# Optimization experiments

Measured on AMD Instinct MI355X. Metric: run time of the kernel, lower is better.

The kernel has to match this reference:

```python
import jax, jax.numpy as jnp
import numpy as np

D = 1024
H = 16
DH = D // H  # 64
FF_H = 4096
EPS = 1e-5


def layernorm(x, gamma, beta):
    mu = jnp.mean(x, axis=-1, keepdims=True)
    var = jnp.var(x, axis=-1, keepdims=True)
    return (x - mu) * jax.lax.rsqrt(var + EPS) * gamma + beta


def setup_inputs() -> dict:
    key = jax.random.key(0)
    ks = jax.random.split(key, 12)
    B, S = 2, 2048
    q = jax.random.normal(ks[0], (B, S, D), dtype=jnp.float32)
    k = jax.random.normal(ks[1], (B, S, D), dtype=jnp.float32)
    v = jax.random.normal(ks[2], (B, S, D), dtype=jnp.float32)
    time_lengths = jax.random.randint(ks[3], (B,), 0, S)
    mask = jnp.zeros((1, 1, S, S), dtype=jnp.float32)
    sc = 0.02
    Wq = jax.random.normal(ks[4], (D, D), dtype=jnp.float32) * sc
    Wk = jax.random.normal(ks[5], (D, D), dtype=jnp.float32) * sc
    Wv = jax.random.normal(ks[6], (D, D), dtype=jnp.float32) * sc
    Wd = jax.random.normal(ks[7], (D, D), dtype=jnp.float32) * sc
    W1 = jax.random.normal(ks[8], (D, FF_H), dtype=jnp.float32) * sc
    b1 = jnp.zeros((FF_H,), dtype=jnp.float32)
    W2 = jax.random.normal(ks[9], (FF_H, D), dtype=jnp.float32) * sc
    b2 = jnp.zeros((D,), dtype=jnp.float32)
    g1 = jnp.ones((D,), dtype=jnp.float32)
    be1 = jnp.zeros((D,), dtype=jnp.float32)
    g2 = jnp.ones((D,), dtype=jnp.float32)
    be2 = jnp.zeros((D,), dtype=jnp.float32)
    return {"q": q, "k": k, "v": v, "time_lengths": time_lengths, "mask": mask,
            "Wq": Wq, "Wk": Wk, "Wv": Wv, "Wd": Wd,
            "W1": W1, "b1": b1, "W2": W2, "b2": b2,
            "g1": g1, "be1": be1, "g2": g2, "be2": be2}


def reference(q, k, v, time_lengths, mask, Wq, Wk, Wv, Wd, W1, b1, W2, b2, g1, be1, g2, be2):
    B, S, _ = q.shape
    scale = jnp.sqrt(jnp.float32(DH))
    # project and split heads: [B,H,S,DH]
    qh = (q @ Wq).reshape(B, S, H, DH).transpose(0, 2, 1, 3)
    kh = (k @ Wk).reshape(B, S, H, DH).transpose(0, 2, 1, 3)
    vh = (v @ Wv).reshape(B, S, H, DH).transpose(0, 2, 1, 3)
    score = jnp.einsum('bhqd,bhkd->bhqk', qh, kh) / scale + mask
    attn = jax.nn.softmax(score, axis=-1)
    z = jnp.einsum('bhqk,bhkd->bhqd', attn, vh)
    z = z.transpose(0, 2, 1, 3).reshape(B, S, D)
    z = z @ Wd
    # Add & LayerNorm 1 (note: original applies LN to attn out, then adds q)
    x = layernorm(z, g1, be1) + q
    # FF (dropout is identity in eval)
    ff = jax.nn.relu(x @ W1 + b1) @ W2 + b2
    return layernorm(ff + x, g2, be2)
```

## Files before the change

### kernel.cpp

```cpp
#include <hip/hip_runtime.h>
#include <hip/hip_bf16.h>


#define SEQ 2048
#define DM  1024
#define LNEPS 1e-5f

typedef __attribute__((ext_vector_type(8))) short bf16x8;
typedef __attribute__((ext_vector_type(4))) float f32x4;

#define GAS __attribute__((address_space(1)))
#define LAS __attribute__((address_space(3)))

static __device__ __forceinline__ void gl_lds16(const unsigned short* g, unsigned short* l) {
    __builtin_amdgcn_global_load_lds((const GAS void*)g, (LAS void*)l, 16, 0, 0);
}

static __device__ __forceinline__ unsigned short f2bf(float f) {
    unsigned u = __builtin_bit_cast(unsigned, f);
    u += 0x7fffu + ((u >> 16) & 1u);
    return (unsigned short)(u >> 16);
}

__global__ __launch_bounds__(256) void gemm_bf16(
    const unsigned short* __restrict__ A, const unsigned short* __restrict__ Bt,
    float* __restrict__ Cf, unsigned short* __restrict__ Cb,
    int M, int N, int Klen, int lda, int ldb,
    size_t sA, size_t sB, size_t sC,
    const float* __restrict__ bias, int ep)
{
    __shared__ unsigned short As[128 * 32];
    __shared__ unsigned short Bs[128 * 32];

    const int t = threadIdx.x, lane = t & 63, w = t >> 6;
    const int wm = w >> 1, wn = w & 1;
    const int m0 = blockIdx.y * 128, n0 = blockIdx.x * 128;
    A  += (size_t)blockIdx.z * sA;
    Bt += (size_t)blockIdx.z * sB;
    const size_t cbase = (size_t)blockIdx.z * sC;
    const int l15 = lane & 15, l16 = lane >> 4;
    const int ar = lane >> 2, ac = (lane & 3) * 8;

    f32x4 acc[4][4];
    #pragma unroll
    for (int i = 0; i < 4; i++)
        #pragma unroll
        for (int j = 0; j < 4; j++)
            acc[i][j] = (f32x4){0.f, 0.f, 0.f, 0.f};

    for (int k0 = 0; k0 < Klen; k0 += 32) {
        __syncthreads();
        #pragma unroll
        for (int i = 0; i < 2; i++) {
            const int rg = w * 2 + i;
            gl_lds16(&A [(size_t)(m0 + rg * 16 + ar) * lda + k0 + ac], &As[rg * 512]);
            gl_lds16(&Bt[(size_t)(n0 + rg * 16 + ar) * ldb + k0 + ac], &Bs[rg * 512]);
        }
        __syncthreads();

        bf16x8 af[4], bfr[4];
        #pragma unroll
        for (int i = 0; i < 4; i++) {
            af[i]  = *(const bf16x8*)&As[(wm * 64 + i * 16 + l15) * 32 + l16 * 8];
            bfr[i] = *(const bf16x8*)&Bs[(wn * 64 + i * 16 + l15) * 32 + l16 * 8];
        }
        #pragma unroll
        for (int mi = 0; mi < 4; mi++)
            #pragma unroll
            for (int ni = 0; ni < 4; ni++)
                acc[mi][ni] = __builtin_amdgcn_mfma_f32_16x16x32_bf16(
                    af[mi], bfr[ni], acc[mi][ni], 0, 0, 0);
    }

    #pragma unroll
    for (int ni = 0; ni < 4; ni++) {
        const int col = n0 + wn * 64 + ni * 16 + l15;
        const float bv = (ep && blockIdx.z == 0) ? bias[col] : 0.f;
        #pragma unroll
        for (int mi = 0; mi < 4; mi++) {
            #pragma unroll
            for (int r = 0; r < 4; r++) {
                const int row = m0 + wm * 64 + mi * 16 + l16 * 4 + r;
                float vv = acc[mi][ni][r] + bv;
                if (ep == 2) vv = fmaxf(vv, 0.f);
                if (Cf) Cf[cbase + (size_t)row * N + col] = vv;
                else    Cb[cbase + (size_t)row * N + col] = f2bf(vv);
            }
        }
    }
}

__global__ __launch_bounds__(256) void attn_mfma(
    const unsigned short* __restrict__ qh, const unsigned short* __restrict__ kh,
    const unsigned short* __restrict__ vhT, const float* __restrict__ mask,
    unsigned short* __restrict__ z)
{
    __shared__ unsigned short Qs[64 * 64];
    __shared__ unsigned short Ks[64 * 64];
    __shared__ unsigned short Vst[64 * 64];
    __shared__ unsigned short Ps[64 * 72];

    const int t = threadIdx.x, lane = t & 63, w = t >> 6;
    const int bid = blockIdx.x;
    const int qt = bid >> 5, h = bid & 15, b = (bid >> 4) & 1;
    const int q0 = qt * 64, qr = w * 16;
    const int l15 = lane & 15, l16 = lane >> 4;

    const int lr = lane >> 3;
    const int gc = ((lane & 7) ^ lr) * 8;

    const size_t qbase = (size_t)(b * SEQ + q0) * DM + h * 64;
    const size_t kbase = (size_t)(b * SEQ) * DM + h * 64;
    const size_t vbase = (size_t)((b * 16 + h) * 64) * SEQ;

    #pragma unroll
    for (int i = 0; i < 2; i++) {
        const int rg = w * 2 + i;
        gl_lds16(&qh[qbase + (size_t)(rg * 8 + lr) * DM + gc], &Qs[rg * 512]);
    }
    __syncthreads();

    const int sw0 = ((l16    ) ^ (l15 & 7)) * 8;
    const int sw1 = ((l16 + 4) ^ (l15 & 7)) * 8;
    const bf16x8 bQ0 = *(const bf16x8*)&Qs[(qr + l15) * 64 + sw0];
    const bf16x8 bQ1 = *(const bf16x8*)&Qs[(qr + l15) * 64 + sw1];

    const float* mrow = mask + (size_t)(q0 + qr + l15) * SEQ;

    float m_i = -1e30f, l_i = 0.f;
    f32x4 o4[4];
    #pragma unroll
    for (int mi = 0; mi < 4; mi++) o4[mi] = (f32x4){0.f, 0.f, 0.f, 0.f};

    for (int kt = 0; kt < SEQ / 64; kt++) {
        const int k0 = kt * 64;
        __syncthreads();
        #pragma unroll
        for (int i = 0; i < 2; i++) {
            const int rg = w * 2 + i;
            gl_lds16(&kh [kbase + (size_t)(k0 + rg * 8 + lr) * DM + gc], &Ks[rg * 512]);
            gl_lds16(&vhT[vbase + (size_t)(rg * 8 + lr) * SEQ + k0 + gc], &Vst[rg * 512]);
        }
        __syncthreads();

        f32x4 s4[4];
        #pragma unroll
        for (int ki = 0; ki < 4; ki++) {
            const int r = ki * 16 + l15;
            const bf16x8 aK0 = *(const bf16x8*)&Ks[r * 64 + sw0];
            const bf16x8 aK1 = *(const bf16x8*)&Ks[r * 64 + sw1];
            f32x4 a0 = (f32x4){0.f, 0.f, 0.f, 0.f};
            a0 = __builtin_amdgcn_mfma_f32_16x16x32_bf16(aK0, bQ0, a0, 0, 0, 0);
            s4[ki] = __builtin_amdgcn_mfma_f32_16x16x32_bf16(aK1, bQ1, a0, 0, 0, 0);
        }

        float sv[4][4];
        #pragma unroll
        for (int ki = 0; ki < 4; ki++) {
            const float4 mv = *(const float4*)&mrow[k0 + ki * 16 + l16 * 4];
            sv[ki][0] = s4[ki][0] * 0.125f + mv.x;
            sv[ki][1] = s4[ki][1] * 0.125f + mv.y;
            sv[ki][2] = s4[ki][2] * 0.125f + mv.z;
            sv[ki][3] = s4[ki][3] * 0.125f + mv.w;
        }

        float rm = -1e30f;
        #pragma unroll
        for (int ki = 0; ki < 4; ki++)
            #pragma unroll
            for (int r = 0; r < 4; r++) rm = fmaxf(rm, sv[ki][r]);
        rm = fmaxf(rm, __shfl_xor(rm, 16));
        rm = fmaxf(rm, __shfl_xor(rm, 32));
        const float mnew  = fmaxf(m_i, rm);
        const float alpha = __expf(m_i - mnew);
        m_i = mnew;

        float ps = 0.f;
        #pragma unroll
        for (int ki = 0; ki < 4; ki++) {
            float p[4];
            #pragma unroll
            for (int r = 0; r < 4; r++) { p[r] = __expf(sv[ki][r] - mnew); ps += p[r]; }
            ushort4 pk;
            pk.x = f2bf(p[0]); pk.y = f2bf(p[1]); pk.z = f2bf(p[2]); pk.w = f2bf(p[3]);
            *(ushort4*)&Ps[(qr + l15) * 72 + ki * 16 + l16 * 4] = pk;
        }
        ps += __shfl_xor(ps, 16);
        ps += __shfl_xor(ps, 32);
        l_i = l_i * alpha + ps;
        #pragma unroll
        for (int mi = 0; mi < 4; mi++)
            #pragma unroll
            for (int r = 0; r < 4; r++) o4[mi][r] *= alpha;

        const bf16x8 bP0 = *(const bf16x8*)&Ps[(qr + l15) * 72 + l16 * 8];
        const bf16x8 bP1 = *(const bf16x8*)&Ps[(qr + l15) * 72 + 32 + l16 * 8];
        #pragma unroll
        for (int mi = 0; mi < 4; mi++) {
            const int r = mi * 16 + l15;
            const bf16x8 aV0 = *(const bf16x8*)&Vst[r * 64 + sw0];
            const bf16x8 aV1 = *(const bf16x8*)&Vst[r * 64 + sw1];
            o4[mi] = __builtin_amdgcn_mfma_f32_16x16x32_bf16(aV0, bP0, o4[mi], 0, 0, 0);
            o4[mi] = __builtin_amdgcn_mfma_f32_16x16x32_bf16(aV1, bP1, o4[mi], 0, 0, 0);
        }
    }

    const float inv = 1.f / l_i;
    #pragma unroll
    for (int mi = 0; mi < 4; mi++) {
        ushort4 ok;
        ok.x = f2bf(o4[mi][0] * inv); ok.y = f2bf(o4[mi][1] * inv);
        ok.z = f2bf(o4[mi][2] * inv); ok.w = f2bf(o4[mi][3] * inv);
        *(ushort4*)&z[(size_t)(b * SEQ + q0 + qr + l15) * DM + h * 64 + mi * 16 + l16 * 4] = ok;
    }
}

__global__ __launch_bounds__(256) void cast3_bf16(
    const float* __restrict__ a0, const float* __restrict__ a1, const float* __restrict__ a2,
    unsigned short* __restrict__ out)
{
    const float* src = blockIdx.z == 0 ? a0 : (blockIdx.z == 1 ? a1 : a2);
    const size_t i = ((size_t)blockIdx.x * 256 + threadIdx.x) * 4;
    const float4 v = *(const float4*)&src[i];
    ushort4 o; o.x = f2bf(v.x); o.y = f2bf(v.y); o.z = f2bf(v.z); o.w = f2bf(v.w);
    *(ushort4*)&out[(size_t)blockIdx.z * ((size_t)SEQ * 2 * DM) + i] = o;
}

__global__ __launch_bounds__(256) void transpose_cast(
    const float* __restrict__ W, unsigned short* __restrict__ Wt, int K, int N)
{
    __shared__ float ts[64][65];
    const int n0 = blockIdx.x * 64, k0 = blockIdx.y * 64;
    const int t = threadIdx.x, r = t >> 4, c4 = (t & 15) * 4;
    #pragma unroll
    for (int i = 0; i < 4; i++) {
        const float4 v = *(const float4*)&W[(size_t)(k0 + r + i * 16) * N + n0 + c4];
        ts[r + i * 16][c4 + 0] = v.x; ts[r + i * 16][c4 + 1] = v.y;
        ts[r + i * 16][c4 + 2] = v.z; ts[r + i * 16][c4 + 3] = v.w;
    }
    __syncthreads();
    #pragma unroll
    for (int i = 0; i < 4; i++) {
        const int n = r + i * 16;
        ushort4 o;
        o.x = f2bf(ts[c4 + 0][n]); o.y = f2bf(ts[c4 + 1][n]);
        o.z = f2bf(ts[c4 + 2][n]); o.w = f2bf(ts[c4 + 3][n]);
        *(ushort4*)&Wt[(size_t)(n0 + n) * K + k0 + c4] = o;
    }
}

__global__ __launch_bounds__(256) void transpose_v(
    const unsigned short* __restrict__ vh, unsigned short* __restrict__ vhT)
{
    __shared__ unsigned short ts[64][80];
    const int s0 = blockIdx.x * 64, h = blockIdx.y, b = blockIdx.z;
    const int t = threadIdx.x, rr = t >> 3, c8 = (t & 7) * 8;
    #pragma unroll
    for (int i = 0; i < 2; i++) {
        const int srow = rr + i * 32;
        *(uint4*)&ts[srow][c8] = *(const uint4*)&vh[(size_t)(b * SEQ + s0 + srow) * DM + h * 64 + c8];
    }
    __syncthreads();
    #pragma unroll
    for (int i = 0; i < 2; i++) {
        const int dr = rr + i * 32;
        ushort4 ov0, ov1;
        ov0.x = ts[c8 + 0][dr]; ov0.y = ts[c8 + 1][dr];
        ov0.z = ts[c8 + 2][dr]; ov0.w = ts[c8 + 3][dr];
        ov1.x = ts[c8 + 4][dr]; ov1.y = ts[c8 + 5][dr];
        ov1.z = ts[c8 + 6][dr]; ov1.w = ts[c8 + 7][dr];
        *(ushort4*)&vhT[(size_t)((b * 16 + h) * 64 + dr) * SEQ + s0 + c8] = ov0;
        *(ushort4*)&vhT[(size_t)((b * 16 + h) * 64 + dr) * SEQ + s0 + c8 + 4] = ov1;
    }
}

__global__ __launch_bounds__(256) void ln_res(
    const float* __restrict__ a, const float* __restrict__ a2,
    const float* __restrict__ r,
    const float* __restrict__ g, const float* __restrict__ be,
    float* __restrict__ out, unsigned short* __restrict__ outb, int mode)
{
    __shared__ float redls[8];
    const int row = blockIdx.x, t = threadIdx.x;
    const size_t base = (size_t)row * DM;

    float vals[4], s = 0.f, sq = 0.f;
    #pragma unroll
    for (int i = 0; i < 4; i++) {
        const int c = t + 256 * i;
        float x = a[base + c];
        if (a2) x += a2[base + c];
        if (mode == 1) x += r[base + c];
        vals[i] = x; s += x; sq += x * x;
    }
    #pragma unroll
    for (int off = 32; off > 0; off >>= 1) { s += __shfl_down(s, off); sq += __shfl_down(sq, off); }
    if ((t & 63) == 0) { redls[t >> 6] = s; redls[4 + (t >> 6)] = sq; }
    __syncthreads();
    s  = redls[0] + redls[1] + redls[2] + redls[3];
    sq = redls[4] + redls[5] + redls[6] + redls[7];

    const float mu  = s * (1.f / 1024.f);
    const float var = sq * (1.f / 1024.f) - mu * mu;
    const float rs  = rsqrtf(var + LNEPS);
    #pragma unroll
    for (int i = 0; i < 4; i++) {
        const int c = t + 256 * i;
        float y = (vals[i] - mu) * rs * g[c] + be[c];
        if (mode == 0) y += r[base + c];
        out[base + c] = y;
        if (outb) outb[base + c] = f2bf(y);
    }
}

extern "C" void kernel_launch(void* const* d_in, const int* in_sizes, int n_in,
                              void* d_out, int out_size, void* d_ws, size_t ws_size,
                              hipStream_t stream)
{
    const float* q    = (const float*)d_in[0];
    const float* k    = (const float*)d_in[1];
    const float* v    = (const float*)d_in[2];
    const float* mask = (const float*)d_in[4];
    const float* Wq   = (const float*)d_in[5];
    const float* Wk   = (const float*)d_in[6];
    const float* Wv   = (const float*)d_in[7];
    const float* Wd   = (const float*)d_in[8];
    const float* W1   = (const float*)d_in[9];
    const float* b1   = (const float*)d_in[10];
    const float* W2   = (const float*)d_in[11];
    const float* b2   = (const float*)d_in[12];
    const float* g1   = (const float*)d_in[13];
    const float* be1  = (const float*)d_in[14];
    const float* g2   = (const float*)d_in[15];
    const float* be2  = (const float*)d_in[16];
    float* out = (float*)d_out;

    char* WS = (char*)d_ws;
    const size_t MiB = 1u << 20;
    const size_t ND  = (size_t)4096 * 1024;

    unsigned short* qb  = (unsigned short*)(WS + 0);
    unsigned short* vhT = (unsigned short*)(WS + 0);
    unsigned short* zb  = (unsigned short*)(WS + 8 * MiB);
    unsigned short* xb  = (unsigned short*)(WS + 16 * MiB);
    unsigned short* Wqt = (unsigned short*)(WS + 24 * MiB);
    unsigned short* Wdt = (unsigned short*)(WS + 30 * MiB);
    unsigned short* W1t = (unsigned short*)(WS + 32 * MiB);
    unsigned short* W2t = (unsigned short*)(WS + 40 * MiB);
    unsigned short* qh  = (unsigned short*)(WS + 48 * MiB);
    float*          zd0 = (float*)(WS + 48 * MiB);
    float*          zd1 = (float*)(WS + 64 * MiB);
    float*          x   = (float*)(WS + 80 * MiB);
    unsigned short* h1  = (unsigned short*)(WS + 96 * MiB);
    float*          y0  = (float*)(WS + 48 * MiB);
    float*          y1  = (float*)(WS + 64 * MiB);

    unsigned short* kh = qh + ND;
    unsigned short* vh = qh + 2 * ND;

    const dim3 blk(256);

    cast3_bf16<<<dim3(4096, 1, 3), blk, 0, stream>>>(q, k, v, qb);
    transpose_cast<<<dim3(16, 16), blk, 0, stream>>>(Wq, Wqt,                   1024, 1024);
    transpose_cast<<<dim3(16, 16), blk, 0, stream>>>(Wk, Wqt + 1024 * 1024,     1024, 1024);
    transpose_cast<<<dim3(16, 16), blk, 0, stream>>>(Wv, Wqt + 2 * 1024 * 1024, 1024, 1024);
    transpose_cast<<<dim3(16, 16), blk, 0, stream>>>(Wd, Wdt, 1024, 1024);
    transpose_cast<<<dim3(64, 16), blk, 0, stream>>>(W1, W1t, 1024, 4096);
    transpose_cast<<<dim3(16, 64), blk, 0, stream>>>(W2, W2t, 4096, 1024);

    gemm_bf16<<<dim3(8, 32, 3), blk, 0, stream>>>(qb, Wqt, nullptr, qh,
        4096, 1024, 1024, 1024, 1024, ND, (size_t)1024 * 1024, ND, nullptr, 0);

    transpose_v<<<dim3(32, 16, 2), blk, 0, stream>>>(vh, vhT);

    attn_mfma<<<dim3(1024), blk, 0, stream>>>(qh, kh, vhT, mask, zb);

    gemm_bf16<<<dim3(8, 32, 2), blk, 0, stream>>>(zb, Wdt, zd0, nullptr,
        4096, 1024, 512, 1024, 1024, 512, 512, ND, nullptr, 0);

    ln_res<<<dim3(4096), blk, 0, stream>>>(zd0, zd1, q, g1, be1, x, xb, 0);

    gemm_bf16<<<dim3(32, 32, 1), blk, 0, stream>>>(xb, W1t, nullptr, h1,
        4096, 4096, 1024, 1024, 1024, 0, 0, 0, b1, 2);
    gemm_bf16<<<dim3(8, 32, 2), blk, 0, stream>>>(h1, W2t, y0, nullptr,
        4096, 1024, 2048, 4096, 4096, 2048, 2048, ND, b2, 1);

    ln_res<<<dim3(4096), blk, 0, stream>>>(y0, y1, x, g2, be2, out, nullptr, 1);
}
```

Before: 504.0 us.

## Double-buffer K tiles in attention with manual vmcnt waits and split barriers

```diff
diff --git a/kernel.cpp b/kernel.cpp
--- a/kernel.cpp
+++ b/kernel.cpp
@@ -95,8 +95,8 @@
     const unsigned short* __restrict__ vhT, const float* __restrict__ mask,
     unsigned short* __restrict__ z)
 {
-    __shared__ unsigned short Qs[64 * 64];
-    __shared__ unsigned short Ks[64 * 64];
+    __shared__ unsigned short Ks0[64 * 64];
+    __shared__ unsigned short Ks1[64 * 64];
     __shared__ unsigned short Vst[64 * 64];
     __shared__ unsigned short Ps[64 * 72];
 
@@ -116,14 +116,16 @@
     #pragma unroll
     for (int i = 0; i < 2; i++) {
         const int rg = w * 2 + i;
-        gl_lds16(&qh[qbase + (size_t)(rg * 8 + lr) * DM + gc], &Qs[rg * 512]);
+        gl_lds16(&qh[qbase + (size_t)(rg * 8 + lr) * DM + gc], &Ks1[rg * 512]);
+        gl_lds16(&kh[kbase + (size_t)(rg * 8 + lr) * DM + gc], &Ks0[rg * 512]);
     }
     __syncthreads();
 
     const int sw0 = ((l16    ) ^ (l15 & 7)) * 8;
     const int sw1 = ((l16 + 4) ^ (l15 & 7)) * 8;
-    const bf16x8 bQ0 = *(const bf16x8*)&Qs[(qr + l15) * 64 + sw0];
-    const bf16x8 bQ1 = *(const bf16x8*)&Qs[(qr + l15) * 64 + sw1];
+    const bf16x8 bQ0 = *(const bf16x8*)&Ks1[(qr + l15) * 64 + sw0];
+    const bf16x8 bQ1 = *(const bf16x8*)&Ks1[(qr + l15) * 64 + sw1];
+    __syncthreads();
 
     const float* mrow = mask + (size_t)(q0 + qr + l15) * SEQ;
 
@@ -134,34 +136,53 @@
 
     for (int kt = 0; kt < SEQ / 64; kt++) {
         const int k0 = kt * 64;
-        __syncthreads();
+        const int kn = ((kt + 1) & (SEQ / 64 - 1)) * 64;
+        unsigned short* Kcur = (kt & 1) ? Ks1 : Ks0;
+        unsigned short* Knxt = (kt & 1) ? Ks0 : Ks1;
+
+        __builtin_amdgcn_s_barrier();
+
+        float4 mv[4];
+        #pragma unroll
+        for (int ki = 0; ki < 4; ki++)
+            mv[ki] = *(const float4*)&mrow[k0 + ki * 16 + l16 * 4];
+
         #pragma unroll
         for (int i = 0; i < 2; i++) {
             const int rg = w * 2 + i;
-            gl_lds16(&kh [kbase + (size_t)(k0 + rg * 8 + lr) * DM + gc], &Ks[rg * 512]);
             gl_lds16(&vhT[vbase + (size_t)(rg * 8 + lr) * SEQ + k0 + gc], &Vst[rg * 512]);
         }
-        __syncthreads();
+        __builtin_amdgcn_sched_barrier(0);
+        #pragma unroll
+        for (int i = 0; i < 2; i++) {
+            const int rg = w * 2 + i;
+            gl_lds16(&kh[kbase + (size_t)(kn + rg * 8 + lr) * DM + gc], &Knxt[rg * 512]);
+        }
+
+        asm volatile("s_waitcnt vmcnt(8)" ::: "memory");
+        __builtin_amdgcn_s_barrier();
+        __builtin_amdgcn_sched_barrier(0);
 
         f32x4 s4[4];
+        __builtin_amdgcn_s_setprio(1);
         #pragma unroll
         for (int ki = 0; ki < 4; ki++) {
             const int r = ki * 16 + l15;
-            const bf16x8 aK0 = *(const bf16x8*)&Ks[r * 64 + sw0];
-            const bf16x8 aK1 = *(const bf16x8*)&Ks[r * 64 + sw1];
+            const bf16x8 aK0 = *(const bf16x8*)&Kcur[r * 64 + sw0];
+            const bf16x8 aK1 = *(const bf16x8*)&Kcur[r * 64 + sw1];
             f32x4 a0 = (f32x4){0.f, 0.f, 0.f, 0.f};
             a0 = __builtin_amdgcn_mfma_f32_16x16x32_bf16(aK0, bQ0, a0, 0, 0, 0);
             s4[ki] = __builtin_amdgcn_mfma_f32_16x16x32_bf16(aK1, bQ1, a0, 0, 0, 0);
         }
+        __builtin_amdgcn_s_setprio(0);
 
         float sv[4][4];
         #pragma unroll
         for (int ki = 0; ki < 4; ki++) {
-            const float4 mv = *(const float4*)&mrow[k0 + ki * 16 + l16 * 4];
-            sv[ki][0] = s4[ki][0] * 0.125f + mv.x;
-            sv[ki][1] = s4[ki][1] * 0.125f + mv.y;
-            sv[ki][2] = s4[ki][2] * 0.125f + mv.z;
-            sv[ki][3] = s4[ki][3] * 0.125f + mv.w;
+            sv[ki][0] = s4[ki][0] * 0.125f + mv[ki].x;
+            sv[ki][1] = s4[ki][1] * 0.125f + mv[ki].y;
+            sv[ki][2] = s4[ki][2] * 0.125f + mv[ki].z;
+            sv[ki][3] = s4[ki][3] * 0.125f + mv[ki].w;
         }
 
         float rm = -1e30f;
@@ -193,8 +214,13 @@
             #pragma unroll
             for (int r = 0; r < 4; r++) o4[mi][r] *= alpha;
 
+        asm volatile("s_waitcnt vmcnt(2)" ::: "memory");
+        __builtin_amdgcn_s_barrier();
+        __builtin_amdgcn_sched_barrier(0);
+
         const bf16x8 bP0 = *(const bf16x8*)&Ps[(qr + l15) * 72 + l16 * 8];
         const bf16x8 bP1 = *(const bf16x8*)&Ps[(qr + l15) * 72 + 32 + l16 * 8];
+        __builtin_amdgcn_s_setprio(1);
         #pragma unroll
         for (int mi = 0; mi < 4; mi++) {
             const int r = mi * 16 + l15;
@@ -203,7 +229,10 @@
             o4[mi] = __builtin_amdgcn_mfma_f32_16x16x32_bf16(aV0, bP0, o4[mi], 0, 0, 0);
             o4[mi] = __builtin_amdgcn_mfma_f32_16x16x32_bf16(aV1, bP1, o4[mi], 0, 0, 0);
         }
-    }
+        __builtin_amdgcn_s_setprio(0);
+    }
+
+    asm volatile("s_waitcnt vmcnt(0)" ::: "memory");
 
     const float inv = 1.f / l_i;
     #pragma unroll
```

New measurement: 495.8 us. About the same (-1.6%).
